# Performance work log

Measured on AMD Instinct MI355X. Metric: run time of the kernel, lower is better.

Reference implementation:

```python
import jax, jax.numpy as jnp
import numpy as np
import math

N, DS, DV, R, B = 65536, 256, 64, 64, 8
H = DV  # GVP hidden vector channels = max(vi, vo)
EPS = 1e-8
SCALE = 1.0 / math.sqrt(DS + 3 * DV)  # d_total = scalar_dim + 3*vector_dim


def _gvp(s, v, wh, ws_w, ws_b, wv, wsv_w, wsv_b):
    # full GVP with vector_gate=True, activations=(silu, sigmoid)
    vt = jnp.swapaxes(v, -1, -2)                                  # [N, 3, DV]
    vh = vt @ wh.T                                                # [N, 3, H]
    vn = jnp.sqrt(jnp.clip(jnp.sum(vh * vh, axis=-2), EPS))       # [N, H] norm_no_nan
    s_out = jnp.concatenate([s, vn], axis=-1) @ ws_w.T + ws_b     # [N, DS]
    v_out = jnp.swapaxes(vh @ wv.T, -1, -2)                       # [N, DV, 3]
    gate = jax.nn.sigmoid(s_out) @ wsv_w.T + wsv_b                # vector_act(s) then wsv
    v_out = v_out * jax.nn.sigmoid(gate)[..., None]
    return jax.nn.silu(s_out), v_out


def _gvp_scalar(s, v, wh, ws_w, ws_b):
    # gate_gvp: vo=0, activations=(None, None) -> scalar output only
    vt = jnp.swapaxes(v, -1, -2)
    vh = vt @ wh.T
    vn = jnp.sqrt(jnp.clip(jnp.sum(vh * vh, axis=-2), EPS))
    return jnp.concatenate([s, vn], axis=-1) @ ws_w.T + ws_b


def _layernorm(x, g, b):
    mu = x.mean(-1, keepdims=True)
    var = ((x - mu) ** 2).mean(-1, keepdims=True)
    return (x - mu) / jnp.sqrt(var + 1e-5) * g + b


def setup_inputs() -> dict:
    key = jax.random.key(0)
    ks = jax.random.split(key, 32)

    def lin(k, fo, fi):
        return (jax.random.normal(k, (fo, fi), jnp.float32) / np.sqrt(fi)).astype(jnp.float32)

    inp = {
        'x_s': jax.random.normal(ks[0], (N, DS), jnp.float32),
        'x_v': jax.random.normal(ks[1], (N, DV, 3), jnp.float32),
        'batch_index': jnp.sort(jax.random.randint(ks[2], (N,), 0, B, jnp.int32)),
    }
    i = 3
    for name in ('q', 'k', 'v', 'o'):
        inp[f'{name}_wh'] = lin(ks[i], H, DV)
        inp[f'{name}_ws_w'] = lin(ks[i + 1], DS, DS + H)
        inp[f'{name}_ws_b'] = jnp.zeros((DS,), jnp.float32)
        inp[f'{name}_wv'] = lin(ks[i + 2], DV, H)
        inp[f'{name}_wsv_w'] = lin(ks[i + 3], DV, DS)
        inp[f'{name}_wsv_b'] = jnp.zeros((DV,), jnp.float32)
        i += 4
    inp['comp_w1'] = lin(ks[i], DS, DS)
    inp['comp_b1'] = jnp.zeros((DS,), jnp.float32)
    inp['ln_g'] = jnp.ones((DS,), jnp.float32)
    inp['ln_b'] = jnp.zeros((DS,), jnp.float32)
    inp['comp_w2'] = lin(ks[i + 1], R, DS)
    inp['comp_b2'] = jnp.zeros((R,), jnp.float32)
    inp['g_wh'] = lin(ks[i + 2], H, DV)
    inp['g_ws_w'] = lin(ks[i + 3], DS, DS + H)
    inp['g_ws_b'] = jnp.zeros((DS,), jnp.float32)
    inp['gate_bias'] = jnp.full((DS,), -1.0, jnp.float32)
    return inp


def reference(x_s, x_v, batch_index,
              q_wh, q_ws_w, q_ws_b, q_wv, q_wsv_w, q_wsv_b,
              k_wh, k_ws_w, k_ws_b, k_wv, k_wsv_w, k_wsv_b,
              v_wh, v_ws_w, v_ws_b, v_wv, v_wsv_w, v_wsv_b,
              o_wh, o_ws_w, o_ws_b, o_wv, o_wsv_w, o_wsv_b,
              comp_w1, comp_b1, ln_g, ln_b, comp_w2, comp_b2,
              g_wh, g_ws_w, g_ws_b, gate_bias):
    Q_s, Q_v = _gvp(x_s, x_v, q_wh, q_ws_w, q_ws_b, q_wv, q_wsv_w, q_wsv_b)
    K_s, K_v = _gvp(x_s, x_v, k_wh, k_ws_w, k_ws_b, k_wv, k_wsv_w, k_wsv_b)
    V_s, V_v = _gvp(x_s, x_v, v_wh, v_ws_w, v_ws_b, v_wv, v_wsv_w, v_wsv_b)

    h = _layernorm(x_s @ comp_w1.T + comp_b1, ln_g, ln_b)
    P = jax.nn.softmax(jax.nn.silu(h) @ comp_w2.T + comp_b2, axis=-1)  # [N, R]

    out_s = jnp.zeros_like(x_s)
    out_v = jnp.zeros_like(x_v)
    # per-graph anchor compression + retrieval (B is a small fixed graph count)
    for b in range(B):
        m = (batch_index == b).astype(x_s.dtype)                  # [N]
        Pm = P * m[:, None]                                       # masked soft assignment
        Kbs = Pm.T @ K_s                                          # [R, DS]
        Vbs = Pm.T @ V_s                                          # [R, DS]
        Kbv = jnp.einsum('nr,nvc->rvc', Pm, K_v)                  # [R, DV, 3]
        Vbv = jnp.einsum('nr,nvc->rvc', Pm, V_v)                  # [R, DV, 3]
        logits = (Q_s @ Kbs.T + jnp.einsum('nvc,rvc->nr', Q_v, Kbv)) * SCALE
        attn = jax.nn.softmax(logits, axis=-1)                    # [N, R]
        out_s = out_s + m[:, None] * (attn @ Vbs)
        out_v = out_v + m[:, None, None] * jnp.einsum('nr,rvc->nvc', attn, Vbv)

    gate_s = jax.nn.sigmoid(_gvp_scalar(x_s, x_v, g_wh, g_ws_w, g_ws_b) + gate_bias)
    gate_v = jax.nn.sigmoid(gate_s.mean(-1, keepdims=True))[..., None]
    return _gvp(out_s * gate_s, out_v * gate_v,
                o_wh, o_ws_w, o_ws_b, o_wv, o_wsv_w, o_wsv_b)
```

## Files before the change

### kernel.cpp

```cpp
#include <hip/hip_runtime.h>

typedef unsigned short u16;
typedef __attribute__((ext_vector_type(8))) short bs8;
typedef __attribute__((ext_vector_type(4))) short bs4;
typedef __attribute__((ext_vector_type(4))) float fx4;
#define MFMA16(a,b,c) __builtin_amdgcn_mfma_f32_16x16x32_bf16(a,b,c,0,0,0)

__device__ __forceinline__ float b2f(u16 u){ return __uint_as_float(((unsigned int)u) << 16); }
__device__ __forceinline__ u16 f2b(float f){
  unsigned int x = __float_as_uint(f);
  unsigned int r = (x + 0x7FFFu + ((x >> 16) & 1u)) >> 16;
  return (u16)r;
}
__device__ __forceinline__ float rcpf(float x){ return __builtin_amdgcn_rcpf(x); }
__device__ __forceinline__ float sigm(float x){ return rcpf(1.f+__expf(-x)); }
__device__ __forceinline__ float siluf(float x){ return x*rcpf(1.f+__expf(-x)); }
__device__ __forceinline__ float wsum(float v){
  #pragma unroll
  for (int o=1;o<64;o<<=1) v += __shfl_xor(v, o);
  return v;
}
__device__ __forceinline__ float wmax(float v){
  #pragma unroll
  for (int o=1;o<64;o<<=1) v = fmaxf(v, __shfl_xor(v, o));
  return v;
}
__device__ __forceinline__ bs8 lds8(const u16* ptr){ return *reinterpret_cast<const bs8*>(ptr); }
__device__ __forceinline__ bs8 glb8(const u16* ptr){ return *reinterpret_cast<const bs8*>(ptr); }

#define XSB_P 328
#define XVB_P 72
#define SGB_P 264
#define UBUF_P 68
#define XQ_P 456
#define AT_P 72

struct GP {
  const float* x_s; const float* x_v; const int* bidx;
  const float* wh[5]; const float* ws_w[5]; const float* ws_b[5];
  const float* wv[4]; const float* wsv_w[4]; const float* wsv_b[4];
  const float *w1, *b1, *lng, *lnb, *w2, *b2, *gbias;
  u16 *wsP, *whP, *wvP, *wsvP, *w1P, *w2P;
  float *wsb_f, *wsvb_f, *b1_f, *b2_f, *lng_f, *lnb_f, *gb_f;
  u16 *KP, *VP, *Gs, *PT, *QB;
  float *Gv, *CK, *CV;
  u16 *CKP, *CVP;
  int *bstart;
  float *Qs, *Qv;
};

__global__ __launch_bounds__(256) void kprep(GP p){
  int idx = blockIdx.x*256 + threadIdx.x;
  if (idx < 409600){
    int s=idx/81920, r=idx%81920;
    int ks=r/8192, r2=r%8192, nt=r2/512, r3=r2%512, ln=r3/8, j=r3%8;
    int n=nt*16+(ln&15), k=ks*32+((ln>>4)*8)+j;
    p.wsP[idx] = f2b(p.ws_w[s][n*320+k]); return;
  }
  idx -= 409600;
  if (idx < 20480){
    int s=idx/4096, r=idx%4096;
    int ks=r/2048, r2=r%2048, nt=r2/512, r3=r2%512, ln=r3/8, j=r3%8;
    int h=nt*16+(ln&15), d=ks*32+((ln>>4)*8)+j;
    p.whP[idx] = f2b(p.wh[s][h*64+d]); return;
  }
  idx -= 20480;
  if (idx < 16384){
    int s=idx/4096, r=idx%4096;
    int ks=r/2048, r2=r%2048, nt=r2/512, r3=r2%512, ln=r3/8, j=r3%8;
    int dd=nt*16+(ln&15), hh=ks*32+((ln>>4)*8)+j;
    p.wvP[idx] = f2b(p.wv[s][dd*64+hh]); return;
  }
  idx -= 16384;
  if (idx < 65536){
    int s=idx/16384, r=idx%16384;
    int ks=r/2048, r2=r%2048, nt=r2/512, r3=r2%512, ln=r3/8, j=r3%8;
    int dd=nt*16+(ln&15), i=ks*32+((ln>>4)*8)+j;
    p.wsvP[idx] = f2b(p.wsv_w[s][dd*256+i]); return;
  }
  idx -= 65536;
  if (idx < 65536){
    int ks=idx/8192, r2=idx%8192, nt=r2/512, r3=r2%512, ln=r3/8, j=r3%8;
    int n=nt*16+(ln&15), k=ks*32+((ln>>4)*8)+j;
    p.w1P[idx] = f2b(p.w1[n*256+k]); return;
  }
  idx -= 65536;
  if (idx < 16384){
    int ks=idx/2048, r2=idx%2048, nt=r2/512, r3=r2%512, ln=r3/8, j=r3%8;
    int rr=nt*16+(ln&15), i=ks*32+((ln>>4)*8)+j;
    p.w2P[idx] = f2b(p.w2[rr*256+i]); return;
  }
  idx -= 16384;
  if (idx < 1280){ int s=idx>>8, i=idx&255; p.wsb_f[idx] = p.ws_b[s][i]; return; }
  idx -= 1280;
  if (idx < 256){ int s=idx>>6, d=idx&63; p.wsvb_f[idx] = p.wsv_b[s][d]; return; }
  idx -= 256;
  if (idx < 256){ p.b1_f[idx] = p.b1[idx]; return; }
  idx -= 256;
  if (idx < 64){ p.b2_f[idx] = p.b2[idx]; return; }
  idx -= 64;
  if (idx < 256){ p.lng_f[idx] = p.lng[idx]; return; }
  idx -= 256;
  if (idx < 256){ p.lnb_f[idx] = p.lnb[idx]; return; }
  idx -= 256;
  if (idx < 256){ p.gb_f[idx] = p.gbias[idx]; return; }
  idx -= 256;
  if (idx < 65536){
    if (idx == 0){
      int b0 = p.bidx[0];
      for (int b=0;b<=b0;b++) p.bstart[b]=0;
      int bl = p.bidx[65535];
      for (int b=bl+1;b<=8;b++) p.bstart[b]=65536;
    } else {
      int a = p.bidx[idx-1], c = p.bidx[idx];
      for (int b=a+1;b<=c;b++) p.bstart[b] = idx;
    }
    return;
  }
}

__device__ __forceinline__ void mfma_vh_vn(const u16* whPs, const u16* xvb, u16* vhb2,
                                           u16* xsb, int lane, int w4){
  fx4 a0={0,0,0,0}, a1={0,0,0,0}, a2={0,0,0,0};
  #pragma unroll
  for (int ks=0; ks<2; ks++){
    bs8 b = glb8(whPs + (ks*4+w4)*512 + lane*8);
    bs8 x0 = lds8(xvb + ( 0 + (lane&15))*XVB_P + ks*32 + ((lane>>4)*8));
    bs8 x1 = lds8(xvb + (16 + (lane&15))*XVB_P + ks*32 + ((lane>>4)*8));
    bs8 x2 = lds8(xvb + (32 + (lane&15))*XVB_P + ks*32 + ((lane>>4)*8));
    a0 = MFMA16(x0,b,a0); a1 = MFMA16(x1,b,a1); a2 = MFMA16(x2,b,a2);
  }
  int h = w4*16 + (lane&15);
  int mrow = (lane>>4)*4;
  #pragma unroll
  for (int r=0;r<4;r++){
    vhb2[( 0+mrow+r)*XVB_P + h] = f2b(a0[r]);
    vhb2[(16+mrow+r)*XVB_P + h] = f2b(a1[r]);
    vhb2[(32+mrow+r)*XVB_P + h] = f2b(a2[r]);
    float nv = __builtin_amdgcn_sqrtf(
        fmaxf(a0[r]*a0[r] + a1[r]*a1[r] + a2[r]*a2[r], 1e-8f));
    xsb[(mrow+r)*XSB_P + 256 + h] = f2b(nv);
  }
  __syncthreads();
}

template<int KS>
__device__ __forceinline__ void mfma_sgemm2(const u16* wsPs, const float* bias,
                                            const u16* xsb, int lane, int wave,
                                            fx4 acc[2][2]){
  #pragma unroll
  for (int h=0;h<2;h++)
    #pragma unroll
    for (int t=0;t<2;t++) acc[h][t]=(fx4){0.f,0.f,0.f,0.f};
  const u16* arow0 = xsb + (lane&15)*XSB_P + ((lane>>4)*8);
  const u16* arow1 = arow0 + 16*XSB_P;
  #pragma unroll
  for (int ks=0; ks<KS; ks++){
    bs8 a0 = lds8(arow0 + ks*32);
    bs8 a1 = lds8(arow1 + ks*32);
    bs8 b0 = glb8(wsPs + (ks*16 + wave*2+0)*512 + lane*8);
    bs8 b1 = glb8(wsPs + (ks*16 + wave*2+1)*512 + lane*8);
    acc[0][0]=MFMA16(a0,b0,acc[0][0]); acc[0][1]=MFMA16(a0,b1,acc[0][1]);
    acc[1][0]=MFMA16(a1,b0,acc[1][0]); acc[1][1]=MFMA16(a1,b1,acc[1][1]);
  }
  #pragma unroll
  for (int t=0;t<2;t++){
    float bv = bias[(wave*2+t)*16 + (lane&15)];
    #pragma unroll
    for (int h=0;h<2;h++){
      acc[h][t][0]+=bv; acc[h][t][1]+=bv; acc[h][t][2]+=bv; acc[h][t][3]+=bv;
    }
  }
}

__device__ __forceinline__ fx4 mfma_g64(const u16* bP, const u16* sgb, int lane, int w4){
  fx4 acc = {0.f,0.f,0.f,0.f};
  const u16* arow = sgb + (lane&15)*SGB_P + ((lane>>4)*8);
  #pragma unroll
  for (int ks=0; ks<8; ks++){
    bs8 a = lds8(arow + ks*32);
    bs8 b = glb8(bP + (ks*4 + w4)*512 + lane*8);
    acc = MFMA16(a,b,acc);
  }
  return acc;
}

__device__ __forceinline__ void mfma_wv(const u16* wvPs, const u16* vhb2,
                                        int lane, int w4, fx4 vo[3]){
  vo[0]=(fx4){0.f,0.f,0.f,0.f}; vo[1]=vo[0]; vo[2]=vo[0];
  #pragma unroll
  for (int ks=0; ks<2; ks++){
    bs8 b = glb8(wvPs + (ks*4+w4)*512 + lane*8);
    #pragma unroll
    for (int c=0;c<3;c++){
      bs8 a = lds8(vhb2 + (c*16 + (lane&15))*XVB_P + ks*32 + ((lane>>4)*8));
      vo[c] = MFMA16(a,b,vo[c]);
    }
  }
}

__global__ __launch_bounds__(512, 4) void k1(GP p){
  __shared__ __align__(16) u16 xsb[32*XSB_P];
  __shared__ __align__(16) u16 xvb[96*XVB_P];
  __shared__ __align__(16) u16 vhb2[96*XVB_P];
  __shared__ __align__(16) u16 sgb[32*SGB_P];
  __shared__ float red[2][8][16];
  __shared__ float redb[2][8][16];
  __shared__ float lnp[2][2][16];
  __shared__ float ubuf[32*UBUF_P];
  const int tid = threadIdx.x, lane = tid&63, wave = tid>>6;
  const int w4 = wave&3, hv = wave>>2;
  const int ml = lane&15, gl = lane>>4;
  const int n0 = blockIdx.x * 32;
  u16* xsbH  = xsb  + hv*16*XSB_P;
  u16* xvbH  = xvb  + hv*48*XVB_P;
  u16* vhb2H = vhb2 + hv*48*XVB_P;
  u16* sgbH  = sgb  + hv*16*SGB_P;

  for (int i=tid;i<2048;i+=512){
    int node=i>>6, c4=(i&63)*4;
    float4 v = *reinterpret_cast<const float4*>(p.x_s + (size_t)(n0+node)*256 + c4);
    u16* d = xsb + node*XSB_P + c4;
    d[0]=f2b(v.x); d[1]=f2b(v.y); d[2]=f2b(v.z); d[3]=f2b(v.w);
  }
  for (int i=tid;i<6144;i+=512){
    int row=i>>6, d=i&63;
    int h=row/48, rr=row-48*h, c=rr>>4, nl=rr&15;
    xvb[row*XVB_P+d] = f2b(p.x_v[(size_t)(n0+h*16+nl)*192 + d*3 + c]);
  }
  __syncthreads();

  fx4 acc[2][2];
  #pragma unroll 1
  for (int s=0; s<3; ++s){
    mfma_vh_vn(p.whP + s*4096, xvbH, vhb2H, xsbH, lane, w4);
    mfma_sgemm2<10>(p.wsP + (size_t)s*81920, p.wsb_f + s*256, xsb, lane, wave, acc);
    bs4 stv[2][2];
    #pragma unroll
    for (int h=0;h<2;h++){
      #pragma unroll
      for (int t=0;t<2;t++){
        int ncol=(wave*2+t)*16+ml;
        #pragma unroll
        for (int r=0;r<4;r++){
          int node16=gl*4+r;
          float v=acc[h][t][r];
          float sg=rcpf(1.f+__expf(-v));
          stv[h][t][r]=(short)f2b(v*sg);
          sgb[(h*16+node16)*SGB_P+ncol]=f2b(sg);
        }
      }
    }
    __syncthreads();
    if (s==0){
      #pragma unroll
      for (int h=0;h<2;h++)
        #pragma unroll
        for (int t=0;t<2;t++){
          int ncol=(wave*2+t)*16+ml;
          #pragma unroll
          for (int r=0;r<4;r++)
            p.QB[(size_t)(n0+h*16+gl*4+r)*448+ncol]=(u16)stv[h][t][r];
        }
    } else {
      u16* KVp = (s==1)? p.KP : p.VP;
      #pragma unroll
      for (int h=0;h<2;h++)
        #pragma unroll
        for (int t=0;t<2;t++){
          int ncol=(wave*2+t)*16+ml;
          *reinterpret_cast<bs4*>(KVp + ((size_t)((n0>>4)+h)*448 + ncol)*16 + gl*4) = stv[h][t];
        }
    }
    fx4 g = mfma_g64(p.wsvP + s*16384, sgbH, lane, w4);
    fx4 vo[3];
    mfma_wv(p.wvP + s*4096, vhb2H, lane, w4, vo);
    int dout = w4*16+ml;
    const int nb = n0 + hv*16;
    if (s==0){
      #pragma unroll
      for (int r=0;r<4;r++){
        int node=gl*4+r;
        float gg = sigm(g[r] + p.wsvb_f[dout]);
        #pragma unroll
        for (int c=0;c<3;c++)
          p.QB[(size_t)(nb+node)*448 + 256 + c*64 + dout] = f2b(vo[c][r]*gg);
      }
    } else {
      u16* KVp=(s==1)?p.KP:p.VP;
      float gg[4];
      #pragma unroll
      for (int r=0;r<4;r++) gg[r] = sigm(g[r] + p.wsvb_f[s*64+dout]);
      #pragma unroll
      for (int c=0;c<3;c++){
        bs4 st;
        #pragma unroll
        for (int r=0;r<4;r++) st[r]=(short)f2b(vo[c][r]*gg[r]);
        *reinterpret_cast<bs4*>(KVp + ((size_t)((n0>>4)+hv)*448 + 256 + c*64 + dout)*16 + gl*4) = st;
      }
    }
    __syncthreads();
  }

  mfma_vh_vn(p.whP + 3*4096, xvbH, vhb2H, xsbH, lane, w4);
  mfma_sgemm2<10>(p.wsP + (size_t)3*81920, p.wsb_f + 3*256, xsb, lane, wave, acc);
  {
    float psum[2][4] = {{0.f,0.f,0.f,0.f},{0.f,0.f,0.f,0.f}};
    u16 gsv[2][2][4];
    #pragma unroll
    for (int h=0;h<2;h++){
      #pragma unroll
      for (int t=0;t<2;t++){
        int ncol=(wave*2+t)*16+ml;
        float gb = p.gb_f[ncol];
        #pragma unroll
        for (int r=0;r<4;r++){
          float gs = sigm(acc[h][t][r] + gb);
          gsv[h][t][r]=f2b(gs);
          psum[h][r] += gs;
        }
      }
    }
    #pragma unroll
    for (int h=0;h<2;h++)
      #pragma unroll
      for (int r=0;r<4;r++){
        #pragma unroll
        for (int o=1;o<16;o<<=1) psum[h][r] += __shfl_xor(psum[h][r], o);
      }
    if (ml==0){
      #pragma unroll
      for (int h=0;h<2;h++)
        #pragma unroll
        for (int r=0;r<4;r++) red[h][wave][gl*4+r] = psum[h][r];
    }
    __syncthreads();
    #pragma unroll
    for (int h=0;h<2;h++)
      #pragma unroll
      for (int t=0;t<2;t++){
        int ncol=(wave*2+t)*16+ml;
        #pragma unroll
        for (int r=0;r<4;r++)
          p.Gs[(size_t)(n0+h*16+gl*4+r)*256+ncol] = gsv[h][t][r];
      }
    if (tid<32){
      int h=tid>>4, nl=tid&15;
      float s8 = red[h][0][nl]+red[h][1][nl]+red[h][2][nl]+red[h][3][nl]
               + red[h][4][nl]+red[h][5][nl]+red[h][6][nl]+red[h][7][nl];
      p.Gv[n0+tid] = sigm(s8*(1.f/256.f));
    }
    __syncthreads();
  }

  mfma_sgemm2<8>(p.w1P, p.b1_f, xsb, lane, wave, acc);
  {
    float s1[2][4]={{0.f,0.f,0.f,0.f},{0.f,0.f,0.f,0.f}};
    float s2[2][4]={{0.f,0.f,0.f,0.f},{0.f,0.f,0.f,0.f}};
    #pragma unroll
    for (int h=0;h<2;h++)
      #pragma unroll
      for (int t=0;t<2;t++)
        #pragma unroll
        for (int r=0;r<4;r++){ float v=acc[h][t][r]; s1[h][r]+=v; s2[h][r]+=v*v; }
    #pragma unroll
    for (int h=0;h<2;h++)
      #pragma unroll
      for (int r=0;r<4;r++){
        #pragma unroll
        for (int o=1;o<16;o<<=1){ s1[h][r]+=__shfl_xor(s1[h][r],o); s2[h][r]+=__shfl_xor(s2[h][r],o); }
      }
    if (ml==0){
      #pragma unroll
      for (int h=0;h<2;h++)
        #pragma unroll
        for (int r=0;r<4;r++){
          red[h][wave][gl*4+r]=s1[h][r];
          redb[h][wave][gl*4+r]=s2[h][r];
        }
    }
    __syncthreads();
    if (tid<32){
      int h=tid>>4, nl=tid&15;
      float S1=red[h][0][nl]+red[h][1][nl]+red[h][2][nl]+red[h][3][nl]
             + red[h][4][nl]+red[h][5][nl]+red[h][6][nl]+red[h][7][nl];
      float S2=redb[h][0][nl]+redb[h][1][nl]+redb[h][2][nl]+redb[h][3][nl]
             + redb[h][4][nl]+redb[h][5][nl]+redb[h][6][nl]+redb[h][7][nl];
      float mu=S1*(1.f/256.f), var=S2*(1.f/256.f)-mu*mu;
      lnp[h][0][nl]=mu; lnp[h][1][nl]=rsqrtf(var+1e-5f);
    }
    __syncthreads();
    #pragma unroll
    for (int h=0;h<2;h++)
      #pragma unroll
      for (int t=0;t<2;t++){
        int ncol=(wave*2+t)*16+ml;
        float g=p.lng_f[ncol], b=p.lnb_f[ncol];
        #pragma unroll
        for (int r=0;r<4;r++){
          int node16=gl*4+r;
          float hh=(acc[h][t][r]-lnp[h][0][node16])*lnp[h][1][node16]*g + b;
          sgb[(h*16+node16)*SGB_P+ncol]=f2b(siluf(hh));
        }
      }
    __syncthreads();
    fx4 u = mfma_g64(p.w2P, sgbH, lane, w4);
    int rcol = w4*16+ml;
    float b2v = p.b2_f[rcol];
    #pragma unroll
    for (int r=0;r<4;r++)
      ubuf[(hv*16 + gl*4+r)*UBUF_P + rcol] = u[r] + b2v;
    __syncthreads();
    bs4 pt4;
    #pragma unroll
    for (int i=0;i<4;i++){
      int node = wave*4+i;
      float uu = ubuf[node*UBUF_P + lane];
      float m = wmax(uu);
      float e = __expf(uu-m);
      float ss = wsum(e);
      pt4[i] = (short)f2b(e*rcpf(ss));
    }
    *reinterpret_cast<bs4*>(p.PT + ((size_t)((n0>>4)+(wave>>2))*64 + lane)*16 + (wave&3)*4) = pt4;
  }
}

__device__ __forceinline__ bs8 ldfrag(const u16* base, int n8, int row, int stride){
  return *reinterpret_cast<const bs8*>(base + ((size_t)(n8>>4)*stride + row)*16 + (n8&15));
}

__global__ __launch_bounds__(256) void k2(GP p){
  const int bid = blockIdx.x;
  const int bb = bid >> 6;
  const int sv = (bid >> 5) & 1;
  const int sp = bid & 31;
  const int lane = threadIdx.x & 63, wave = threadIdx.x >> 6;
  const int ml = lane & 15, gl = lane >> 4;
  int s0 = p.bstart[bb], s1 = p.bstart[bb+1];
  int len = s1 - s0; if (len <= 0) return;
  int cl = (((len + 31) >> 5) + 7) & ~7;
  int kb0 = s0 + sp*cl; if (kb0 >= s1) return;
  int kb1 = kb0 + cl; if (kb1 > s1) kb1 = s1;
  int kba = kb0 & ~7;
  const u16* F = sv ? p.VP : p.KP;
  fx4 acc[4][7];
  #pragma unroll
  for (int m=0;m<4;m++)
    #pragma unroll
    for (int t=0;t<7;t++) acc[m][t]=(fx4){0.f,0.f,0.f,0.f};

  for (int kb = kba; kb < kb1; kb += 32){
    int n8 = kb + gl*8;
    bool edge = (kb < kb0) | (kb + 32 > kb1);
    bs8 a[4];
    #pragma unroll
    for (int m=0;m<4;m++) a[m] = ldfrag(p.PT, n8, m*16+ml, 64);
    if (edge){
      #pragma unroll
      for (int j=0;j<8;j++){
        int n = n8 + j;
        if (n < kb0 || n >= kb1){
          #pragma unroll
          for (int m=0;m<4;m++) a[m][j]=0;
        }
      }
    }
    #pragma unroll
    for (int t=0;t<7;t++){
      bs8 bf = ldfrag(F, n8, (wave*7+t)*16+ml, 448);
      if (edge){
        #pragma unroll
        for (int j=0;j<8;j++){
          int n = n8 + j;
          if (n < kb0 || n >= kb1) bf[j]=0;
        }
      }
      #pragma unroll
      for (int m=0;m<4;m++) acc[m][t] = MFMA16(a[m], bf, acc[m][t]);
    }
  }
  #pragma unroll
  for (int m=0;m<4;m++){
    #pragma unroll
    for (int t=0;t<7;t++){
      int f = (wave*7+t)*16 + ml;
      int r0 = m*16 + gl*4;
      if (sv==0){
        float* dst = p.CK + ((size_t)bb*448+f)*64 + r0;
        #pragma unroll
        for (int j=0;j<4;j++) atomicAdd(dst+j, acc[m][t][j]);
      } else {
        float* dst = p.CV + ((size_t)bb*64+r0)*448 + f;
        #pragma unroll
        for (int j=0;j<4;j++) atomicAdd(dst + (size_t)j*448, acc[m][t][j]);
      }
    }
  }
}

__global__ __launch_bounds__(256) void k2b(GP p){
  int idx = blockIdx.x*256 + threadIdx.x;
  if (idx < 229376){
    int b=idx/28672, r=idx%28672;
    int ks=r/2048, r2=r%2048, nt=r2/512, r3=r2%512, ln=r3/8, j=r3&7;
    int f=ks*32+((ln>>4)*8)+j, rr=nt*16+(ln&15);
    p.CKP[idx] = f2b(p.CK[((size_t)b*448+f)*64+rr] * 0.047245559f);
    return;
  }
  idx -= 229376;
  int b=idx/28672, r=idx%28672;
  int ks=r/14336, r2=r%14336, nt=r2/512, r3=r2%512, ln=r3/8, j=r3&7;
  int rr=ks*32+((ln>>4)*8)+j, f=nt*16+(ln&15);
  p.CVP[idx] = f2b(p.CV[((size_t)b*64+rr)*448+f]);
}

__global__ __launch_bounds__(512, 4) void k3(GP p){
  __shared__ __align__(16) char smem[68608];
  u16* xq   = (u16*)smem;
  u16* atb  = (u16*)(smem+29184);
  u16* xsb  = (u16*)(smem+33792);
  u16* xvb  = (u16*)(smem+54784);
  u16* vhb2 = (u16*)smem;
  u16* sgb  = (u16*)(smem+13824);
  __shared__ float redm[2][4][16];
  __shared__ float reds[2][4][16];
  __shared__ int Bl[32];
  const int tid = threadIdx.x;
  const int n0 = blockIdx.x * 32;
  const int lane = tid & 63, wave = tid >> 6;
  const int w4 = wave&3, hv = wave>>2;
  const int ml = lane&15, gl = lane>>4;
  const int nb = n0 + hv*16;
  u16* xqH   = xq   + hv*16*XQ_P;
  u16* atbH  = atb  + hv*16*AT_P;
  u16* xsbH  = xsb  + hv*16*XSB_P;
  u16* xvbH  = xvb  + hv*48*XVB_P;
  u16* vhb2H = vhb2 + hv*48*XVB_P;
  u16* sgbH  = sgb  + hv*16*SGB_P;
  const int* BlH = Bl + hv*16;

  for (int idx=tid; idx<1792; idx+=512){
    int node = idx/56, q = idx-node*56;
    bs8 v = *reinterpret_cast<const bs8*>(p.QB + (size_t)(n0+node)*448 + q*8);
    *reinterpret_cast<bs8*>(xq + node*XQ_P + q*8) = v;
  }
  if (tid<32) Bl[tid] = p.bidx[n0+tid];
  __syncthreads();

  int bb = Bl[0];
  while (true){
    fx4 lac = {0.f,0.f,0.f,0.f};
    {
      const u16* ckb = p.CKP + (size_t)bb*28672;
      const u16* arow = xqH + ml*XQ_P + gl*8;
      #pragma unroll
      for (int ks=0; ks<14; ks++){
        bs8 a = lds8(arow + ks*32);
        bs8 b = glb8(ckb + (ks*4+w4)*512 + lane*8);
        lac = MFMA16(a,b,lac);
      }
    }
    float loc[4];
    #pragma unroll
    for (int r=0;r<4;r++){
      float m = lac[r];
      #pragma unroll
      for (int o=1;o<16;o<<=1) m = fmaxf(m, __shfl_xor(m,o));
      loc[r]=m;
    }
    if (ml==0){
      #pragma unroll
      for (int r=0;r<4;r++) redm[hv][w4][gl*4+r]=loc[r];
    }
    __syncthreads();
    float e4[4];
    #pragma unroll
    for (int r=0;r<4;r++){
      int node=gl*4+r;
      float gm = fmaxf(fmaxf(redm[hv][0][node],redm[hv][1][node]),
                       fmaxf(redm[hv][2][node],redm[hv][3][node]));
      float e = __expf(lac[r]-gm);
      e4[r]=e;
      float s=e;
      #pragma unroll
      for (int o=1;o<16;o<<=1) s += __shfl_xor(s,o);
      loc[r]=s;
    }
    if (ml==0){
      #pragma unroll
      for (int r=0;r<4;r++) reds[hv][w4][gl*4+r]=loc[r];
    }
    __syncthreads();
    #pragma unroll
    for (int r=0;r<4;r++){
      int node=gl*4+r;
      float tot = reds[hv][0][node]+reds[hv][1][node]+reds[hv][2][node]+reds[hv][3][node];
      atbH[node*AT_P + w4*16 + ml] = f2b(e4[r]*rcpf(tot));
    }
    __syncthreads();
    {
      const u16* cvb = p.CVP + (size_t)bb*28672;
      const u16* prow = atbH + ml*AT_P + gl*8;
      bs8 a0 = lds8(prow);
      bs8 a1 = lds8(prow + 32);
      #pragma unroll
      for (int t=0;t<7;t++){
        int nt = w4*7 + t;
        fx4 pv = {0.f,0.f,0.f,0.f};
        pv = MFMA16(a0, glb8(cvb + nt*512 + lane*8), pv);
        pv = MFMA16(a1, glb8(cvb + (28+nt)*512 + lane*8), pv);
        int f = nt*16 + ml;
        #pragma unroll
        for (int r=0;r<4;r++){
          int node=gl*4+r;
          if (BlH[node]!=bb) continue;
          if (f < 256){
            xsbH[node*XSB_P+f] = f2b(pv[r]);
          } else {
            int fm=f-256, c=fm>>6, d=fm&63;
            xvbH[(c*16+node)*XVB_P+d] = f2b(pv[r]);
          }
        }
      }
    }
    int nxt = 0x7fffffff;
    #pragma unroll
    for (int i=0;i<32;i++){ int v=Bl[i]; if (v>bb && v<nxt) nxt=v; }
    if (nxt==0x7fffffff) break;
    bb = nxt;
    __syncthreads();
  }
  __syncthreads();

  for (int i=tid; i<1024; i+=512){
    int node=i>>5, f8=(i&31)*8;
    bs8 g8 = *reinterpret_cast<const bs8*>(p.Gs + (size_t)(n0+node)*256 + f8);
    u16* xp = xsb + node*XSB_P + f8;
    bs8 x8 = *reinterpret_cast<bs8*>(xp);
    bs8 o8;
    #pragma unroll
    for (int j=0;j<8;j++)
      o8[j] = (short)f2b(b2f((u16)x8[j]) * b2f((u16)g8[j]));
    *reinterpret_cast<bs8*>(xp) = o8;
  }
  for (int i=tid; i<768; i+=512){
    int node=i/24, g=i-node*24;
    int fm=g*8, c=fm>>6, d=fm&63;
    int row=(node>>4)*48 + c*16 + (node&15);
    float gv = p.Gv[n0+node];
    u16* xp = xvb + row*XVB_P + d;
    bs8 x8 = *reinterpret_cast<bs8*>(xp);
    bs8 o8;
    #pragma unroll
    for (int j=0;j<8;j++)
      o8[j] = (short)f2b(b2f((u16)x8[j]) * gv);
    *reinterpret_cast<bs8*>(xp) = o8;
  }
  __syncthreads();

  mfma_vh_vn(p.whP + 4*4096, xvbH, vhb2H, xsbH, lane, w4);
  fx4 acc[2][2];
  mfma_sgemm2<10>(p.wsP + (size_t)4*81920, p.wsb_f + 4*256, xsb, lane, wave, acc);
  #pragma unroll
  for (int h=0;h<2;h++){
    #pragma unroll
    for (int t=0;t<2;t++){
      int ncol=(wave*2+t)*16+ml;
      #pragma unroll
      for (int r=0;r<4;r++){
        int node16=gl*4+r;
        float v=acc[h][t][r];
        float sg=rcpf(1.f+__expf(-v));
        p.Qs[(size_t)(n0+h*16+node16)*256+ncol]=v*sg;
        sgb[(h*16+node16)*SGB_P+ncol]=f2b(sg);
      }
    }
  }
  __syncthreads();
  fx4 g = mfma_g64(p.wsvP + 3*16384, sgbH, lane, w4);
  fx4 vo[3];
  mfma_wv(p.wvP + 3*4096, vhb2H, lane, w4, vo);
  int dout = w4*16+ml;
  #pragma unroll
  for (int r=0;r<4;r++){
    int node=gl*4+r;
    float gg = sigm(g[r] + p.wsvb_f[3*64+dout]);
    #pragma unroll
    for (int c=0;c<3;c++)
      p.Qv[(size_t)(nb+node)*192 + dout*3 + c] = vo[c][r]*gg;
  }
}

extern "C" void kernel_launch(void* const* d_in, const int* in_sizes, int n_in,
                              void* d_out, int out_size, void* d_ws, size_t ws_size,
                              hipStream_t stream){
  (void)in_sizes; (void)n_in; (void)out_size; (void)ws_size;
  GP p;
  p.x_s  = (const float*)d_in[0];
  p.x_v  = (const float*)d_in[1];
  p.bidx = (const int*)d_in[2];
  const int whI[5]  = {3, 9, 15, 33, 21};
  const int wswI[5] = {4, 10, 16, 34, 22};
  const int wsbI[5] = {5, 11, 17, 35, 23};
  const int wvI[4]  = {6, 12, 18, 24};
  const int wsvwI[4]= {7, 13, 19, 25};
  const int wsvbI[4]= {8, 14, 20, 26};
  for (int s=0;s<5;s++){
    p.wh[s]   = (const float*)d_in[whI[s]];
    p.ws_w[s] = (const float*)d_in[wswI[s]];
    p.ws_b[s] = (const float*)d_in[wsbI[s]];
  }
  for (int s=0;s<4;s++){
    p.wv[s]    = (const float*)d_in[wvI[s]];
    p.wsv_w[s] = (const float*)d_in[wsvwI[s]];
    p.wsv_b[s] = (const float*)d_in[wsvbI[s]];
  }
  p.w1    = (const float*)d_in[27];
  p.b1    = (const float*)d_in[28];
  p.lng   = (const float*)d_in[29];
  p.lnb   = (const float*)d_in[30];
  p.w2    = (const float*)d_in[31];
  p.b2    = (const float*)d_in[32];
  p.gbias = (const float*)d_in[36];

  char* w = (char*)d_ws;
  auto alloc = [&](size_t bytes)->char*{
    char* r = w; w += (bytes + 255) & ~(size_t)255; return r;
  };
  p.wsP   = (u16*)alloc(409600u*2);
  p.whP   = (u16*)alloc(20480u*2);
  p.wvP   = (u16*)alloc(16384u*2);
  p.wsvP  = (u16*)alloc(65536u*2);
  p.w1P   = (u16*)alloc(65536u*2);
  p.w2P   = (u16*)alloc(16384u*2);
  p.wsb_f  = (float*)alloc(1280u*4);
  p.wsvb_f = (float*)alloc(256u*4);
  p.b1_f   = (float*)alloc(256u*4);
  p.b2_f   = (float*)alloc(64u*4);
  p.lng_f  = (float*)alloc(256u*4);
  p.lnb_f  = (float*)alloc(256u*4);
  p.gb_f   = (float*)alloc(256u*4);
  p.QB = (u16*)alloc((size_t)65536*448*2);
  p.KP = (u16*)alloc((size_t)65536*448*2 + (1u<<22));
  p.VP = (u16*)alloc((size_t)65536*448*2 + (1u<<22));
  p.Gs = (u16*)alloc((size_t)65536*256*2);
  p.PT = (u16*)alloc((size_t)65536*64*2 + (1u<<20));
  p.Gv = (float*)alloc((size_t)65536*4);
  p.CK = (float*)alloc((size_t)8*448*64*4);
  p.CV = (float*)alloc((size_t)8*448*64*4);
  p.CKP = (u16*)alloc((size_t)8*448*64*2);
  p.CVP = (u16*)alloc((size_t)8*448*64*2);
  p.bstart = (int*)alloc(64);
  p.Qs = (float*)d_out;
  p.Qv = (float*)d_out + (size_t)65536*256;

  hipMemsetAsync(p.CK, 0, (size_t)8*448*64*4, stream);
  hipMemsetAsync(p.CV, 0, (size_t)8*448*64*4, stream);
  kprep<<<2587, 256, 0, stream>>>(p);
  k1<<<2048, 512, 0, stream>>>(p);
  k2<<<512, 256, 0, stream>>>(p);
  k2b<<<1792, 256, 0, stream>>>(p);
  k3<<<2048, 512, 0, stream>>>(p);
}
```

Baseline: 687.0 us.

## Double k1 node tile to 64 per 1024-thread block, reusing weight fragments

k1 now handles 64 nodes per block with 16 waves instead of 32 nodes with 8 waves. In the new scalar GEMM helper, each wave loads one weight fragment per K step and applies it to four 16-node row tiles, so global weight reads per node are halved. The reduction, layernorm and softmax scratch buffers now share LDS with the vh buffer to hold down shared-memory growth. The price is larger blocks, more LDS per block, wider reductions and possibly lower occupancy.

```diff
diff --git a/kernel.cpp b/kernel.cpp
--- a/kernel.cpp
+++ b/kernel.cpp
@@ -145,6 +145,30 @@
 }
 
 template<int KS>
+__device__ __forceinline__ void mfma_sgemm4(const u16* wsPs, const float* bias,
+                                            const u16* xsb_, int lane, int wave,
+                                            fx4 acc[4]){
+  #pragma unroll
+  for (int h=0;h<4;h++) acc[h]=(fx4){0.f,0.f,0.f,0.f};
+  const u16* arow = xsb_ + (lane&15)*XSB_P + ((lane>>4)*8);
+  #pragma unroll
+  for (int ks=0; ks<KS; ks++){
+    bs8 b0 = glb8(wsPs + (ks*16 + wave)*512 + lane*8);
+    bs8 a0 = lds8(arow + ks*32);
+    bs8 a1 = lds8(arow + 16*XSB_P + ks*32);
+    bs8 a2 = lds8(arow + 32*XSB_P + ks*32);
+    bs8 a3 = lds8(arow + 48*XSB_P + ks*32);
+    acc[0]=MFMA16(a0,b0,acc[0]); acc[1]=MFMA16(a1,b0,acc[1]);
+    acc[2]=MFMA16(a2,b0,acc[2]); acc[3]=MFMA16(a3,b0,acc[3]);
+  }
+  float bv = bias[wave*16 + (lane&15)];
+  #pragma unroll
+  for (int h=0;h<4;h++){
+    acc[h][0]+=bv; acc[h][1]+=bv; acc[h][2]+=bv; acc[h][3]+=bv;
+  }
+}
+
+template<int KS>
 __device__ __forceinline__ void mfma_sgemm2(const u16* wsPs, const float* bias,
                                             const u16* xsb, int lane, int wave,
                                             fx4 acc[2][2]){
@@ -199,78 +223,66 @@
   }
 }
 
-__global__ __launch_bounds__(512, 4) void k1(GP p){
-  __shared__ __align__(16) u16 xsb[32*XSB_P];
-  __shared__ __align__(16) u16 xvb[96*XVB_P];
-  __shared__ __align__(16) u16 vhb2[96*XVB_P];
-  __shared__ __align__(16) u16 sgb[32*SGB_P];
-  __shared__ float red[2][8][16];
-  __shared__ float redb[2][8][16];
-  __shared__ float lnp[2][2][16];
-  __shared__ float ubuf[32*UBUF_P];
+__global__ __launch_bounds__(1024, 4) void k1(GP p){
+  __shared__ __align__(16) u16 xsb[64*XSB_P];
+  __shared__ __align__(16) u16 xvb[192*XVB_P];
+  __shared__ __align__(16) u16 vhb2[192*XVB_P];
+  __shared__ __align__(16) u16 sgb[64*SGB_P];
+  float* ubuf = (float*)vhb2;
+  float (*red)[16][16]  = (float(*)[16][16])((char*)vhb2 + 17408);
+  float (*redb)[16][16] = (float(*)[16][16])((char*)vhb2 + 21504);
+  float (*lnp)[2][16]   = (float(*)[2][16])((char*)vhb2 + 25600);
   const int tid = threadIdx.x, lane = tid&63, wave = tid>>6;
   const int w4 = wave&3, hv = wave>>2;
   const int ml = lane&15, gl = lane>>4;
-  const int n0 = blockIdx.x * 32;
+  const int n0 = blockIdx.x * 64;
   u16* xsbH  = xsb  + hv*16*XSB_P;
   u16* xvbH  = xvb  + hv*48*XVB_P;
   u16* vhb2H = vhb2 + hv*48*XVB_P;
   u16* sgbH  = sgb  + hv*16*SGB_P;
 
-  for (int i=tid;i<2048;i+=512){
+  for (int i=tid;i<4096;i+=1024){
     int node=i>>6, c4=(i&63)*4;
     float4 v = *reinterpret_cast<const float4*>(p.x_s + (size_t)(n0+node)*256 + c4);
     u16* d = xsb + node*XSB_P + c4;
     d[0]=f2b(v.x); d[1]=f2b(v.y); d[2]=f2b(v.z); d[3]=f2b(v.w);
   }
-  for (int i=tid;i<6144;i+=512){
+  for (int i=tid;i<12288;i+=1024){
     int row=i>>6, d=i&63;
     int h=row/48, rr=row-48*h, c=rr>>4, nl=rr&15;
     xvb[row*XVB_P+d] = f2b(p.x_v[(size_t)(n0+h*16+nl)*192 + d*3 + c]);
   }
   __syncthreads();
 
-  fx4 acc[2][2];
+  fx4 acc[4];
   #pragma unroll 1
   for (int s=0; s<3; ++s){
     mfma_vh_vn(p.whP + s*4096, xvbH, vhb2H, xsbH, lane, w4);
-    mfma_sgemm2<10>(p.wsP + (size_t)s*81920, p.wsb_f + s*256, xsb, lane, wave, acc);
-    bs4 stv[2][2];
-    #pragma unroll
-    for (int h=0;h<2;h++){
-      #pragma unroll
-      for (int t=0;t<2;t++){
-        int ncol=(wave*2+t)*16+ml;
-        #pragma unroll
-        for (int r=0;r<4;r++){
-          int node16=gl*4+r;
-          float v=acc[h][t][r];
-          float sg=rcpf(1.f+__expf(-v));
-          stv[h][t][r]=(short)f2b(v*sg);
-          sgb[(h*16+node16)*SGB_P+ncol]=f2b(sg);
-        }
+    mfma_sgemm4<10>(p.wsP + (size_t)s*81920, p.wsb_f + s*256, xsb, lane, wave, acc);
+    int ncol = wave*16 + ml;
+    bs4 stv[4];
+    #pragma unroll
+    for (int h=0;h<4;h++){
+      #pragma unroll
+      for (int r=0;r<4;r++){
+        float v=acc[h][r];
+        float sg=rcpf(1.f+__expf(-v));
+        stv[h][r]=(short)f2b(v*sg);
+        sgb[(h*16+gl*4+r)*SGB_P+ncol]=f2b(sg);
       }
     }
     __syncthreads();
     if (s==0){
       #pragma unroll
-      for (int h=0;h<2;h++)
-        #pragma unroll
-        for (int t=0;t<2;t++){
-          int ncol=(wave*2+t)*16+ml;
-          #pragma unroll
-          for (int r=0;r<4;r++)
-            p.QB[(size_t)(n0+h*16+gl*4+r)*448+ncol]=(u16)stv[h][t][r];
-        }
+      for (int h=0;h<4;h++)
+        #pragma unroll
+        for (int r=0;r<4;r++)
+          p.QB[(size_t)(n0+h*16+gl*4+r)*448+ncol]=(u16)stv[h][r];
     } else {
       u16* KVp = (s==1)? p.KP : p.VP;
       #pragma unroll
-      for (int h=0;h<2;h++)
-        #pragma unroll
-        for (int t=0;t<2;t++){
-          int ncol=(wave*2+t)*16+ml;
-          *reinterpret_cast<bs4*>(KVp + ((size_t)((n0>>4)+h)*448 + ncol)*16 + gl*4) = stv[h][t];
-        }
+      for (int h=0;h<4;h++)
+        *reinterpret_cast<bs4*>(KVp + ((size_t)((n0>>4)+h)*448 + ncol)*16 + gl*4) = stv[h];
     }
     fx4 g = mfma_g64(p.wsvP + s*16384, sgbH, lane, w4);
     fx4 vo[3];
@@ -303,68 +315,59 @@
   }
 
   mfma_vh_vn(p.whP + 3*4096, xvbH, vhb2H, xsbH, lane, w4);
-  mfma_sgemm2<10>(p.wsP + (size_t)3*81920, p.wsb_f + 3*256, xsb, lane, wave, acc);
+  mfma_sgemm4<10>(p.wsP + (size_t)3*81920, p.wsb_f + 3*256, xsb, lane, wave, acc);
   {
-    float psum[2][4] = {{0.f,0.f,0.f,0.f},{0.f,0.f,0.f,0.f}};
-    u16 gsv[2][2][4];
-    #pragma unroll
-    for (int h=0;h<2;h++){
-      #pragma unroll
-      for (int t=0;t<2;t++){
-        int ncol=(wave*2+t)*16+ml;
-        float gb = p.gb_f[ncol];
-        #pragma unroll
-        for (int r=0;r<4;r++){
-          float gs = sigm(acc[h][t][r] + gb);
-          gsv[h][t][r]=f2b(gs);
-          psum[h][r] += gs;
-        }
-      }
-    }
-    #pragma unroll
-    for (int h=0;h<2;h++)
+    int ncol = wave*16 + ml;
+    float gb = p.gb_f[ncol];
+    float psum[4][4];
+    u16 gsv[4][4];
+    #pragma unroll
+    for (int h=0;h<4;h++)
       #pragma unroll
       for (int r=0;r<4;r++){
+        float gs = sigm(acc[h][r] + gb);
+        gsv[h][r]=f2b(gs);
+        psum[h][r]=gs;
+      }
+    #pragma unroll
+    for (int h=0;h<4;h++)
+      #pragma unroll
+      for (int r=0;r<4;r++){
         #pragma unroll
         for (int o=1;o<16;o<<=1) psum[h][r] += __shfl_xor(psum[h][r], o);
       }
     if (ml==0){
       #pragma unroll
-      for (int h=0;h<2;h++)
+      for (int h=0;h<4;h++)
         #pragma unroll
         for (int r=0;r<4;r++) red[h][wave][gl*4+r] = psum[h][r];
     }
     __syncthreads();
     #pragma unroll
-    for (int h=0;h<2;h++)
-      #pragma unroll
-      for (int t=0;t<2;t++){
-        int ncol=(wave*2+t)*16+ml;
-        #pragma unroll
-        for (int r=0;r<4;r++)
-          p.Gs[(size_t)(n0+h*16+gl*4+r)*256+ncol] = gsv[h][t][r];
-      }
-    if (tid<32){
+    for (int h=0;h<4;h++)
+      #pragma unroll
+      for (int r=0;r<4;r++)
+        p.Gs[(size_t)(n0+h*16+gl*4+r)*256+ncol] = gsv[h][r];
+    if (tid<64){
       int h=tid>>4, nl=tid&15;
-      float s8 = red[h][0][nl]+red[h][1][nl]+red[h][2][nl]+red[h][3][nl]
-               + red[h][4][nl]+red[h][5][nl]+red[h][6][nl]+red[h][7][nl];
-      p.Gv[n0+tid] = sigm(s8*(1.f/256.f));
-    }
-    __syncthreads();
-  }
-
-  mfma_sgemm2<8>(p.w1P, p.b1_f, xsb, lane, wave, acc);
+      float s16=0.f;
+      #pragma unroll
+      for (int w=0;w<16;w++) s16 += red[h][w][nl];
+      p.Gv[n0+tid] = sigm(s16*(1.f/256.f));
+    }
+    __syncthreads();
+  }
+
+  mfma_sgemm4<8>(p.w1P, p.b1_f, xsb, lane, wave, acc);
   {
-    float s1[2][4]={{0.f,0.f,0.f,0.f},{0.f,0.f,0.f,0.f}};
-    float s2[2][4]={{0.f,0.f,0.f,0.f},{0.f,0.f,0.f,0.f}};
-    #pragma unroll
-    for (int h=0;h<2;h++)
-      #pragma unroll
-      for (int t=0;t<2;t++)
-        #pragma unroll
-        for (int r=0;r<4;r++){ float v=acc[h][t][r]; s1[h][r]+=v; s2[h][r]+=v*v; }
-    #pragma unroll
-    for (int h=0;h<2;h++)
+    int ncol = wave*16 + ml;
+    float s1[4][4], s2[4][4];
+    #pragma unroll
+    for (int h=0;h<4;h++)
+      #pragma unroll
+      for (int r=0;r<4;r++){ float v=acc[h][r]; s1[h][r]=v; s2[h][r]=v*v; }
+    #pragma unroll
+    for (int h=0;h<4;h++)
       #pragma unroll
       for (int r=0;r<4;r++){
         #pragma unroll
@@ -372,7 +375,7 @@
       }
     if (ml==0){
       #pragma unroll
-      for (int h=0;h<2;h++)
+      for (int h=0;h<4;h++)
         #pragma unroll
         for (int r=0;r<4;r++){
           red[h][wave][gl*4+r]=s1[h][r];
@@ -380,28 +383,23 @@
         }
     }
     __syncthreads();
-    if (tid<32){
+    if (tid<64){
       int h=tid>>4, nl=tid&15;
-      float S1=red[h][0][nl]+red[h][1][nl]+red[h][2][nl]+red[h][3][nl]
-             + red[h][4][nl]+red[h][5][nl]+red[h][6][nl]+red[h][7][nl];
-      float S2=redb[h][0][nl]+redb[h][1][nl]+redb[h][2][nl]+redb[h][3][nl]
-             + redb[h][4][nl]+redb[h][5][nl]+redb[h][6][nl]+redb[h][7][nl];
+      float S1=0.f, S2=0.f;
+      #pragma unroll
+      for (int w=0;w<16;w++){ S1+=red[h][w][nl]; S2+=redb[h][w][nl]; }
       float mu=S1*(1.f/256.f), var=S2*(1.f/256.f)-mu*mu;
       lnp[h][0][nl]=mu; lnp[h][1][nl]=rsqrtf(var+1e-5f);
     }
     __syncthreads();
-    #pragma unroll
-    for (int h=0;h<2;h++)
-      #pragma unroll
-      for (int t=0;t<2;t++){
-        int ncol=(wave*2+t)*16+ml;
-        float g=p.lng_f[ncol], b=p.lnb_f[ncol];
-        #pragma unroll
-        for (int r=0;r<4;r++){
-          int node16=gl*4+r;
-          float hh=(acc[h][t][r]-lnp[h][0][node16])*lnp[h][1][node16]*g + b;
-          sgb[(h*16+node16)*SGB_P+ncol]=f2b(siluf(hh));
-        }
+    float g=p.lng_f[ncol], b=p.lnb_f[ncol];
+    #pragma unroll
+    for (int h=0;h<4;h++)
+      #pragma unroll
+      for (int r=0;r<4;r++){
+        int node16=gl*4+r;
+        float hh=(acc[h][r]-lnp[h][0][node16])*lnp[h][1][node16]*g + b;
+        sgb[(h*16+node16)*SGB_P+ncol]=f2b(siluf(hh));
       }
     __syncthreads();
     fx4 u = mfma_g64(p.w2P, sgbH, lane, w4);
@@ -757,7 +755,7 @@
   hipMemsetAsync(p.CK, 0, (size_t)8*448*64*4, stream);
   hipMemsetAsync(p.CV, 0, (size_t)8*448*64*4, stream);
   kprep<<<2587, 256, 0, stream>>>(p);
-  k1<<<2048, 512, 0, stream>>>(p);
+  k1<<<1024, 1024, 0, stream>>>(p);
   k2<<<512, 256, 0, stream>>>(p);
   k2b<<<1792, 256, 0, stream>>>(p);
   k3<<<2048, 512, 0, stream>>>(p);
```

New measurement: 760.8 us. +10.7%, slower.
